# Kernel optimization log

Hardware: AMD Instinct MI355X
Metric: run time of the kernel (lower is better)

Reference implementation:

```python
import jax, jax.numpy as jnp
import numpy as np

NUM_STUDENTS = 50000
NUM_KP = 100
KD = 128          # knowledge_dim
HID = 256         # hidden_dim
B = 16384
K = 20            # max_knowledge_points


def setup_inputs() -> dict:
    key = jax.random.key(0)
    ks = jax.random.split(key, 16)
    inp = {
        "student_indices": jax.random.randint(ks[0], (B,), 0, NUM_STUDENTS, dtype=jnp.int32),
        "kp_indices": jax.random.randint(ks[1], (B, K), 0, NUM_KP, dtype=jnp.int32),
        "kp_lengths": jax.random.randint(ks[2], (B,), 0, K + 1, dtype=jnp.int32),
        # learned parameters
        "emb": jax.random.normal(ks[3], (NUM_STUDENTS, NUM_KP, KD), dtype=jnp.float32),
        # attention: Linear(KD,HID) -> tanh -> Linear(HID,1) -> softmax(dim=1)
        "W1": jax.random.normal(ks[4], (KD, HID), dtype=jnp.float32) * 0.05,
        "b1": jnp.zeros((HID,), jnp.float32),
        "w2": jax.random.normal(ks[5], (HID, 1), dtype=jnp.float32) * 0.05,
        "b2": jnp.zeros((1,), jnp.float32),
        # MLP: Linear(KD,HID)-ReLU-Linear(HID,HID//2)-ReLU-Linear(HID//2,1)-Sigmoid
        "M1": jax.random.normal(ks[6], (KD, HID), dtype=jnp.float32) * 0.05,
        "mb1": jnp.zeros((HID,), jnp.float32),
        "M2": jax.random.normal(ks[7], (HID, HID // 2), dtype=jnp.float32) * 0.05,
        "mb2": jnp.zeros((HID // 2,), jnp.float32),
        "M3": jax.random.normal(ks[8], (HID // 2, 1), dtype=jnp.float32) * 0.05,
        "mb3": jnp.zeros((1,), jnp.float32),
    }
    return inp


def reference(student_indices, kp_indices, kp_lengths, emb, W1, b1, w2, b2,
              M1, mb1, M2, mb2, M3, mb3):
    # ragged gather -> padded [B, K, KD]; padded slots are zero (as in the torch loop)
    vecs = emb[student_indices[:, None], kp_indices]            # [B,K,KD]
    mask = (jnp.arange(K)[None, :] < kp_lengths[:, None]).astype(vecs.dtype)  # [B,K]
    vecs = vecs * mask[:, :, None]
    # attention: Linear-Tanh-Linear-Softmax(dim=1), THEN masked (matches original order)
    logits = jnp.tanh(vecs @ W1 + b1) @ w2 + b2                 # [B,K,1]
    att = jax.nn.softmax(logits, axis=1) * mask[:, :, None]     # [B,K,1]
    weighted = jnp.sum(att * vecs, axis=1)                      # [B,KD]
    # MLP (dropout = identity in eval)
    h = jax.nn.relu(weighted @ M1 + mb1)
    h = jax.nn.relu(h @ M2 + mb2)
    scores = jax.nn.sigmoid(h @ M3 + mb3)[:, 0]                 # [B]
    return scores, att[:, :, 0]
```

## Files before the change

kernel.cpp:

```cpp
#include <hip/hip_runtime.h>
#include <hip/hip_bf16.h>

#define K_ 20
#define KD_ 128
#define HID_ 256
#define NKP_ 100

using short8_t = __attribute__((ext_vector_type(8))) short;
using f32x4 = __attribute__((ext_vector_type(4))) float;

__device__ __forceinline__ unsigned short f2bf(float f) {
    union { __hip_bfloat16 h; unsigned short u; } c; c.h = __float2bfloat16(f); return c.u;
}
__device__ __forceinline__ float vexp(float x) { float r; asm("v_exp_f32 %0, %1" : "=v"(r) : "v"(x)); return r; }
__device__ __forceinline__ float vrcp(float x) { float r; asm("v_rcp_f32 %0, %1" : "=v"(r) : "v"(x)); return r; }
__device__ __forceinline__ float bf_lo(unsigned u) { return __uint_as_float(u << 16); }
__device__ __forceinline__ float bf_hi(unsigned u) { return __uint_as_float(u & 0xffff0000u); }

#define CEXP 2.885390081777927f

__global__ __launch_bounds__(256) void prep_frags(
    const float* __restrict__ W1, const float* __restrict__ M1,
    const float* __restrict__ M2, unsigned short* __restrict__ w1f,
    unsigned short* __restrict__ m1f, unsigned short* __restrict__ m2f)
{
    const int b = blockIdx.x;
    const float* src; unsigned short* dst; int nc, smask, nshift, ib;
    if (b < 128)      { src = W1; dst = w1f; nc = 256; smask = 3; nshift = 2; ib = b; }
    else if (b < 256) { src = M1; dst = m1f; nc = 256; smask = 3; nshift = 2; ib = b - 128; }
    else              { src = M2; dst = m2f; nc = 128; smask = 7; nshift = 3; ib = b - 256; }
    const int i = ib * 256 + threadIdx.x;
    const int j = i & 7, l = (i >> 3) & 63, f = i >> 9;
    const int s = f & smask, n = f >> nshift;
    const int k = s * 32 + (l >> 4) * 8 + j;
    const int col = n * 16 + (l & 15);
    dst[i] = f2bf(src[k * nc + col]);
}

__global__ __launch_bounds__(256, 3) void cdm_attn(
    const int* __restrict__ stu_idx, const int* __restrict__ kp_idx,
    const int* __restrict__ kp_len, const float* __restrict__ emb,
    const unsigned short* __restrict__ w1f,
    const float* __restrict__ b1, const float* __restrict__ w2,
    const float* __restrict__ b2,
    float* __restrict__ out_att, unsigned short* __restrict__ wsum_g)
{
    const int tid = threadIdx.x, lane = tid & 63, w = tid >> 6;
    const int base = blockIdx.x * 8;

    __shared__ unsigned short vec_s[8][K_][KD_];
    __shared__ float lp_s[4][2][4][24];
    __shared__ float l0_s[4];
    __shared__ int   len_s[8];
    __shared__ float att_s[8][K_];

    const int g = lane >> 4, c16 = lane & 15;
    int lens[2]; long long eb[2]; int kpr[2][5];
#pragma unroll
    for (int h = 0; h < 2; ++h) {
        const int gs = base + 2 * w + h;
        lens[h] = kp_len[gs];
        eb[h] = (long long)stu_idx[gs] * (NKP_ * KD_);
#pragma unroll
        for (int it = 0; it < 5; ++it)
            kpr[h][it] = kp_idx[gs * K_ + it * 4 + g];
    }

    {
        float4 va[10], vb[10];
#pragma unroll
        for (int h = 0; h < 2; ++h) {
#pragma unroll
            for (int it = 0; it < 5; ++it) {
                const int q = h * 5 + it;
                va[q] = make_float4(0.f, 0.f, 0.f, 0.f);
                vb[q] = make_float4(0.f, 0.f, 0.f, 0.f);
                const int r = it * 4 + g;
                if (r < lens[h]) {
                    const float4* src = (const float4*)(emb + eb[h] + (long long)kpr[h][it] * KD_) + c16 * 2;
                    va[q] = src[0]; vb[q] = src[1];
                }
            }
        }
#pragma unroll
        for (int h = 0; h < 2; ++h) {
            char* sb = (char*)&vec_s[2 * w + h][0][0];
#pragma unroll
            for (int it = 0; it < 5; ++it) {
                const int q = h * 5 + it;
                const int r = it * 4 + g;
                short8_t pk;
                pk[0] = (short)f2bf(va[q].x); pk[1] = (short)f2bf(va[q].y);
                pk[2] = (short)f2bf(va[q].z); pk[3] = (short)f2bf(va[q].w);
                pk[4] = (short)f2bf(vb[q].x); pk[5] = (short)f2bf(vb[q].y);
                pk[6] = (short)f2bf(vb[q].z); pk[7] = (short)f2bf(vb[q].w);
                *(short8_t*)(sb + r * 256 + ((c16 * 16) ^ ((r & 7) << 4))) = pk;
            }
        }
        if (lane == 0) { len_s[2 * w] = lens[0]; len_s[2 * w + 1] = lens[1]; }
    }

    short8_t Bf[4][4];
    {
        const short8_t* bfr = (const short8_t*)w1f;
#pragma unroll
        for (int nn = 0; nn < 4; ++nn)
#pragma unroll
            for (int s = 0; s < 4; ++s)
                Bf[nn][s] = bfr[((w * 4 + nn) * 4 + s) * 64 + lane];
    }
    float b1C[4], w2r[4], n2r[4];
#pragma unroll
    for (int nn = 0; nn < 4; ++nn) {
        const int c = (w * 4 + nn) * 16 + (lane & 15);
        b1C[nn] = b1[c] * CEXP;
        w2r[nn] = w2[c];
        n2r[nn] = -2.f * w2r[nn];
    }
    const float b2v = b2[0];

    {
        float p = 0.f;
#pragma unroll
        for (int nn = 0; nn < 4; ++nn)
            p = fmaf(n2r[nn], vrcp(vexp(b1C[nn]) + 1.f), p + w2r[nn]);
#pragma unroll
        for (int m = 1; m <= 8; m <<= 1) p += __shfl_xor(p, m);
        if (lane == 0) l0_s[w] = p;
    }
    __syncthreads();
    const float logit0 = l0_s[0] + l0_s[1] + l0_s[2] + l0_s[3] + b2v;

#pragma unroll
    for (int p = 0; p < 4; ++p) {
        const int sp = 2 * p;
        const int lA = len_s[sp], lB = len_s[sp + 1];
        const bool need2 = (lA > 16) || (lB > 16);

        short8_t A0[4], A1[4];
        {
            const char* bA = (const char*)&vec_s[sp][0][0];
            const char* bB = (const char*)&vec_s[sp + 1][0][0];
            const int lr = lane & 15;
            const int rowb = lr * 256;
#pragma unroll
            for (int s = 0; s < 4; ++s) {
                const int colA = (s * 64 + (lane >> 4) * 16) ^ ((lr & 7) << 4);
                A0[s] = *(const short8_t*)(bA + rowb + colA);
                A1[s] = *(const short8_t*)(bB + rowb + colA);
            }
        }

        float lp0[4] = {0, 0, 0, 0}, lp1[4] = {0, 0, 0, 0};
#pragma unroll
        for (int nn = 0; nn < 4; ++nn) {
            f32x4 a0 = {0.f, 0.f, 0.f, 0.f}, a1 = {0.f, 0.f, 0.f, 0.f};
#pragma unroll
            for (int s = 0; s < 4; ++s) {
                a0 = __builtin_amdgcn_mfma_f32_16x16x32_bf16(A0[s], Bf[nn][s], a0, 0, 0, 0);
                a1 = __builtin_amdgcn_mfma_f32_16x16x32_bf16(A1[s], Bf[nn][s], a1, 0, 0, 0);
            }
            const float bc = b1C[nn], wv = w2r[nn], n2 = n2r[nn];
#pragma unroll
            for (int i = 0; i < 4; ++i) {
                lp0[i] = fmaf(n2, vrcp(vexp(fmaf(a0[i], CEXP, bc)) + 1.f), lp0[i] + wv);
                lp1[i] = fmaf(n2, vrcp(vexp(fmaf(a1[i], CEXP, bc)) + 1.f), lp1[i] + wv);
            }
        }
#pragma unroll
        for (int i = 0; i < 4; ++i) {
#pragma unroll
            for (int m = 1; m <= 8; m <<= 1) {
                lp0[i] += __shfl_xor(lp0[i], m);
                lp1[i] += __shfl_xor(lp1[i], m);
            }
        }
        if ((lane & 15) == 0) {
            const int gq = lane >> 4;
#pragma unroll
            for (int i = 0; i < 4; ++i) {
                lp_s[p][0][w][gq * 4 + i] = lp0[i];
                lp_s[p][1][w][gq * 4 + i] = lp1[i];
            }
        }

        if (need2) {
            short8_t A2[4];
            const int lr = lane & 15;
            const char* t2b = (const char*)&vec_s[sp + ((lr >> 2) & 1)][0][0] + (16 + (lr & 3)) * 256;
            const bool v2 = lr < 8;
            const short8_t z = {0, 0, 0, 0, 0, 0, 0, 0};
#pragma unroll
            for (int s = 0; s < 4; ++s) {
                const int colT = s * 64 + (lane >> 4) * 16;
                const short8_t t = *(const short8_t*)(t2b + (colT ^ ((lr & 3) << 4)));
                A2[s] = v2 ? t : z;
            }
            float lp2[4] = {0, 0, 0, 0};
#pragma unroll
            for (int nn = 0; nn < 4; ++nn) {
                f32x4 a2 = {0.f, 0.f, 0.f, 0.f};
#pragma unroll
                for (int s = 0; s < 4; ++s)
                    a2 = __builtin_amdgcn_mfma_f32_16x16x32_bf16(A2[s], Bf[nn][s], a2, 0, 0, 0);
                const float bc = b1C[nn], wv = w2r[nn], n2 = n2r[nn];
#pragma unroll
                for (int i = 0; i < 4; ++i)
                    lp2[i] = fmaf(n2, vrcp(vexp(fmaf(a2[i], CEXP, bc)) + 1.f), lp2[i] + wv);
            }
#pragma unroll
            for (int i = 0; i < 4; ++i) {
#pragma unroll
                for (int m = 1; m <= 8; m <<= 1) lp2[i] += __shfl_xor(lp2[i], m);
            }
            if ((lane & 15) == 0 && (lane >> 4) < 2) {
                const int gq = lane >> 4;
#pragma unroll
                for (int i = 0; i < 4; ++i) lp_s[p][gq][w][16 + i] = lp2[i];
            }
        }
    }
    __syncthreads();

    {
        const int j = lane & 31, hh = lane >> 5;
        const int smp = 2 * w + hh;
        const int gsS = base + smp;
        const int lenS = len_s[smp];
        float logit = -1e30f;
        if (j < K_) {
            logit = (j < lenS)
                ? b2v + lp_s[w][hh][0][j] + lp_s[w][hh][1][j]
                      + lp_s[w][hh][2][j] + lp_s[w][hh][3][j]
                : logit0;
        }
        float mx = logit;
#pragma unroll
        for (int m = 16; m >= 1; m >>= 1) mx = fmaxf(mx, __shfl_xor(mx, m, 32));
        const float e = (j < K_) ? vexp((logit - mx) * 1.44269504f) : 0.f;
        float sm = e;
#pragma unroll
        for (int m = 16; m >= 1; m >>= 1) sm += __shfl_xor(sm, m, 32);
        const float attv = (j < lenS) ? e * vrcp(sm) : 0.f;
        if (j < K_) { att_s[smp][j] = attv; out_att[gsS * K_ + j] = attv; }

        const int d0 = (lane & 31) * 4;
        const char* vb2 = (const char*)&vec_s[smp][0][0];
        const int lm = max(len_s[2 * w], len_s[2 * w + 1]);
        float s0 = 0.f, s1 = 0.f, s2 = 0.f, s3 = 0.f;
        for (int k = 0; k < lm; ++k) {
            const float av = att_s[smp][k];
            const uint2 u = *(const uint2*)(vb2 + k * 256 + ((2 * d0) ^ ((k & 7) << 4)));
            s0 = fmaf(av, bf_lo(u.x), s0);
            s1 = fmaf(av, bf_hi(u.x), s1);
            s2 = fmaf(av, bf_lo(u.y), s2);
            s3 = fmaf(av, bf_hi(u.y), s3);
        }
        uint2 pk;
        pk.x = (unsigned)f2bf(s0) | ((unsigned)f2bf(s1) << 16);
        pk.y = (unsigned)f2bf(s2) | ((unsigned)f2bf(s3) << 16);
        *(uint2*)(wsum_g + gsS * KD_ + d0) = pk;
    }
}

__global__ __launch_bounds__(512) void cdm_mlp(
    const unsigned short* __restrict__ wsum_g,
    const unsigned short* __restrict__ m1f, const unsigned short* __restrict__ m2f,
    const float* __restrict__ mb1, const float* __restrict__ mb2,
    const float* __restrict__ M3, const float* __restrict__ mb3,
    float* __restrict__ out_scores)
{
    const int tid = threadIdx.x, lane = tid & 63, w = tid >> 6;
    const int S0 = blockIdx.x * 32;
    const int lr = lane & 15, g = lane >> 4;

    __shared__ unsigned short h1_s[32][HID_];
    __shared__ float sc_s[8][32];

    short8_t Aw[2][4];
#pragma unroll
    for (int m = 0; m < 2; ++m)
#pragma unroll
        for (int s = 0; s < 4; ++s)
            Aw[m][s] = *(const short8_t*)(wsum_g + (S0 + m * 16 + lr) * KD_
                                          + s * 32 + g * 8);
    short8_t B1r[2][4];
    {
        const short8_t* bf1 = (const short8_t*)m1f;
#pragma unroll
        for (int nn = 0; nn < 2; ++nn)
#pragma unroll
            for (int s = 0; s < 4; ++s)
                B1r[nn][s] = bf1[((w * 2 + nn) * 4 + s) * 64 + lane];
    }
#pragma unroll
    for (int nn = 0; nn < 2; ++nn) {
        f32x4 c0 = {0.f, 0.f, 0.f, 0.f}, c1 = {0.f, 0.f, 0.f, 0.f};
#pragma unroll
        for (int s = 0; s < 4; ++s) {
            c0 = __builtin_amdgcn_mfma_f32_16x16x32_bf16(Aw[0][s], B1r[nn][s], c0, 0, 0, 0);
            c1 = __builtin_amdgcn_mfma_f32_16x16x32_bf16(Aw[1][s], B1r[nn][s], c1, 0, 0, 0);
        }
        const int col = (w * 2 + nn) * 16 + lr;
        const float bias = mb1[col];
#pragma unroll
        for (int i = 0; i < 4; ++i) {
            const int r0 = g * 4 + i;
            const int r1 = 16 + r0;
            *(unsigned short*)((char*)h1_s + r0 * 512 + ((2 * col) ^ ((r0 & 7) << 4)))
                = f2bf(fmaxf(c0[i] + bias, 0.f));
            *(unsigned short*)((char*)h1_s + r1 * 512 + ((2 * col) ^ ((r0 & 7) << 4)))
                = f2bf(fmaxf(c1[i] + bias, 0.f));
        }
    }
    __syncthreads();

    short8_t B2r[8];
    {
        const short8_t* bf2 = (const short8_t*)m2f;
#pragma unroll
        for (int s = 0; s < 8; ++s)
            B2r[s] = bf2[(w * 8 + s) * 64 + lane];
    }
    f32x4 d0 = {0.f, 0.f, 0.f, 0.f}, d1 = {0.f, 0.f, 0.f, 0.f};
#pragma unroll
    for (int s = 0; s < 8; ++s) {
        const int off = (s * 64 + g * 16) ^ ((lr & 7) << 4);
        const short8_t Ah0 = *(const short8_t*)((const char*)h1_s + lr * 512 + off);
        const short8_t Ah1 = *(const short8_t*)((const char*)h1_s + (16 + lr) * 512 + off);
        d0 = __builtin_amdgcn_mfma_f32_16x16x32_bf16(Ah0, B2r[s], d0, 0, 0, 0);
        d1 = __builtin_amdgcn_mfma_f32_16x16x32_bf16(Ah1, B2r[s], d1, 0, 0, 0);
    }
    {
        const int col = w * 16 + lr;
        const float bb = mb2[col], m3v = M3[col];
        float part0[4], part1[4];
#pragma unroll
        for (int i = 0; i < 4; ++i) {
            part0[i] = fmaxf(d0[i] + bb, 0.f) * m3v;
            part1[i] = fmaxf(d1[i] + bb, 0.f) * m3v;
        }
#pragma unroll
        for (int i = 0; i < 4; ++i) {
#pragma unroll
            for (int q = 1; q <= 8; q <<= 1) {
                part0[i] += __shfl_xor(part0[i], q);
                part1[i] += __shfl_xor(part1[i], q);
            }
        }
        if (lr == 0) {
#pragma unroll
            for (int i = 0; i < 4; ++i) {
                sc_s[w][g * 4 + i]      = part0[i];
                sc_s[w][16 + g * 4 + i] = part1[i];
            }
        }
    }
    __syncthreads();
    if (tid < 32) {
        const float sc = sc_s[0][tid] + sc_s[1][tid] + sc_s[2][tid] + sc_s[3][tid]
                       + sc_s[4][tid] + sc_s[5][tid] + sc_s[6][tid] + sc_s[7][tid] + mb3[0];
        out_scores[S0 + tid] = 1.f / (1.f + __expf(-sc));
    }
}

extern "C" void kernel_launch(void* const* d_in, const int* in_sizes, int n_in,
                              void* d_out, int out_size, void* d_ws, size_t ws_size,
                              hipStream_t stream) {
    const int*   stu = (const int*)d_in[0];
    const int*   kpi = (const int*)d_in[1];
    const int*   kpl = (const int*)d_in[2];
    const float* emb = (const float*)d_in[3];
    const float* W1  = (const float*)d_in[4];
    const float* b1  = (const float*)d_in[5];
    const float* w2  = (const float*)d_in[6];
    const float* b2  = (const float*)d_in[7];
    const float* M1  = (const float*)d_in[8];
    const float* mb1 = (const float*)d_in[9];
    const float* M2  = (const float*)d_in[10];
    const float* mb2 = (const float*)d_in[11];
    const float* M3  = (const float*)d_in[12];
    const float* mb3 = (const float*)d_in[13];
    const int B = in_sizes[0];

    float* out_scores = (float*)d_out;
    float* out_att    = out_scores + B;

    unsigned short* w1f  = (unsigned short*)d_ws;
    unsigned short* m1f  = w1f + 32768;
    unsigned short* m2f  = m1f + 32768;
    unsigned short* wsum = m2f + 32768;

    prep_frags<<<384, 256, 0, stream>>>(W1, M1, M2, w1f, m1f, m2f);
    cdm_attn<<<B / 8, 256, 0, stream>>>(stu, kpi, kpl, emb, w1f, b1, w2, b2,
                                        out_att, wsum);
    cdm_mlp<<<B / 32, 512, 0, stream>>>(wsum, m1f, m2f, mb1, mb2, M3, mb3, out_scores);
}
```

Measured before the change: 71.84 us.

## Halve students per attention block and assign one student per wave

The attention kernel now handles 4 students per 256-thread block instead of 8, so each wave gathers and owns a single student. The grid doubles and launch bounds rise to 4 blocks per CU, since shared memory use is halved. The weighted-sum stage now uses a full 64-lane wave per student and loops only up to that student's length instead of the pair maximum. The intent is more blocks in flight to hide gather latency and less wasted work. In exchange, each block reloads the W1 fragments and recomputes logit0 for half as many students, and there is less memory-level parallelism per wave.

```diff
diff --git a/kernel.cpp b/kernel.cpp
--- a/kernel.cpp
+++ b/kernel.cpp
@@ -37,7 +37,7 @@
     dst[i] = f2bf(src[k * nc + col]);
 }
 
-__global__ __launch_bounds__(256, 3) void cdm_attn(
+__global__ __launch_bounds__(256, 4) void cdm_attn(
     const int* __restrict__ stu_idx, const int* __restrict__ kp_idx,
     const int* __restrict__ kp_len, const float* __restrict__ emb,
     const unsigned short* __restrict__ w1f,
@@ -46,58 +46,47 @@
     float* __restrict__ out_att, unsigned short* __restrict__ wsum_g)
 {
     const int tid = threadIdx.x, lane = tid & 63, w = tid >> 6;
-    const int base = blockIdx.x * 8;
-
-    __shared__ unsigned short vec_s[8][K_][KD_];
-    __shared__ float lp_s[4][2][4][24];
+    const int base = blockIdx.x * 4;
+
+    __shared__ unsigned short vec_s[4][K_][KD_];
+    __shared__ float lp_s[2][2][4][24];
     __shared__ float l0_s[4];
-    __shared__ int   len_s[8];
-    __shared__ float att_s[8][K_];
+    __shared__ int   len_s[4];
+    __shared__ float att_s[4][K_];
 
     const int g = lane >> 4, c16 = lane & 15;
-    int lens[2]; long long eb[2]; int kpr[2][5];
-#pragma unroll
-    for (int h = 0; h < 2; ++h) {
-        const int gs = base + 2 * w + h;
-        lens[h] = kp_len[gs];
-        eb[h] = (long long)stu_idx[gs] * (NKP_ * KD_);
-#pragma unroll
-        for (int it = 0; it < 5; ++it)
-            kpr[h][it] = kp_idx[gs * K_ + it * 4 + g];
-    }
-
-    {
-        float4 va[10], vb[10];
-#pragma unroll
-        for (int h = 0; h < 2; ++h) {
-#pragma unroll
-            for (int it = 0; it < 5; ++it) {
-                const int q = h * 5 + it;
-                va[q] = make_float4(0.f, 0.f, 0.f, 0.f);
-                vb[q] = make_float4(0.f, 0.f, 0.f, 0.f);
-                const int r = it * 4 + g;
-                if (r < lens[h]) {
-                    const float4* src = (const float4*)(emb + eb[h] + (long long)kpr[h][it] * KD_) + c16 * 2;
-                    va[q] = src[0]; vb[q] = src[1];
-                }
-            }
-        }
-#pragma unroll
-        for (int h = 0; h < 2; ++h) {
-            char* sb = (char*)&vec_s[2 * w + h][0][0];
-#pragma unroll
-            for (int it = 0; it < 5; ++it) {
-                const int q = h * 5 + it;
-                const int r = it * 4 + g;
-                short8_t pk;
-                pk[0] = (short)f2bf(va[q].x); pk[1] = (short)f2bf(va[q].y);
-                pk[2] = (short)f2bf(va[q].z); pk[3] = (short)f2bf(va[q].w);
-                pk[4] = (short)f2bf(vb[q].x); pk[5] = (short)f2bf(vb[q].y);
-                pk[6] = (short)f2bf(vb[q].z); pk[7] = (short)f2bf(vb[q].w);
-                *(short8_t*)(sb + r * 256 + ((c16 * 16) ^ ((r & 7) << 4))) = pk;
-            }
-        }
-        if (lane == 0) { len_s[2 * w] = lens[0]; len_s[2 * w + 1] = lens[1]; }
+    const int gs = base + w;
+    const int len = kp_len[gs];
+    const long long eb = (long long)stu_idx[gs] * (NKP_ * KD_);
+    int kpr[5];
+#pragma unroll
+    for (int it = 0; it < 5; ++it)
+        kpr[it] = kp_idx[gs * K_ + it * 4 + g];
+
+    {
+        float4 va[5], vb[5];
+#pragma unroll
+        for (int it = 0; it < 5; ++it) {
+            va[it] = make_float4(0.f, 0.f, 0.f, 0.f);
+            vb[it] = make_float4(0.f, 0.f, 0.f, 0.f);
+            const int r = it * 4 + g;
+            if (r < len) {
+                const float4* src = (const float4*)(emb + eb + (long long)kpr[it] * KD_) + c16 * 2;
+                va[it] = src[0]; vb[it] = src[1];
+            }
+        }
+        char* sb = (char*)&vec_s[w][0][0];
+#pragma unroll
+        for (int it = 0; it < 5; ++it) {
+            const int r = it * 4 + g;
+            short8_t pk;
+            pk[0] = (short)f2bf(va[it].x); pk[1] = (short)f2bf(va[it].y);
+            pk[2] = (short)f2bf(va[it].z); pk[3] = (short)f2bf(va[it].w);
+            pk[4] = (short)f2bf(vb[it].x); pk[5] = (short)f2bf(vb[it].y);
+            pk[6] = (short)f2bf(vb[it].z); pk[7] = (short)f2bf(vb[it].w);
+            *(short8_t*)(sb + r * 256 + ((c16 * 16) ^ ((r & 7) << 4))) = pk;
+        }
+        if (lane == 0) len_s[w] = len;
     }
 
     short8_t Bf[4][4];
@@ -132,7 +121,7 @@
     const float logit0 = l0_s[0] + l0_s[1] + l0_s[2] + l0_s[3] + b2v;
 
 #pragma unroll
-    for (int p = 0; p < 4; ++p) {
+    for (int p = 0; p < 2; ++p) {
         const int sp = 2 * p;
         const int lA = len_s[sp], lB = len_s[sp + 1];
         const bool need2 = (lA > 16) || (lB > 16);
@@ -223,43 +212,35 @@
     __syncthreads();
 
     {
-        const int j = lane & 31, hh = lane >> 5;
-        const int smp = 2 * w + hh;
-        const int gsS = base + smp;
-        const int lenS = len_s[smp];
+        const int p = w >> 1, hh = w & 1;
+        const int lenS = len_s[w];
         float logit = -1e30f;
-        if (j < K_) {
-            logit = (j < lenS)
-                ? b2v + lp_s[w][hh][0][j] + lp_s[w][hh][1][j]
-                      + lp_s[w][hh][2][j] + lp_s[w][hh][3][j]
+        if (lane < K_) {
+            logit = (lane < lenS)
+                ? b2v + lp_s[p][hh][0][lane] + lp_s[p][hh][1][lane]
+                      + lp_s[p][hh][2][lane] + lp_s[p][hh][3][lane]
                 : logit0;
         }
         float mx = logit;
 #pragma unroll
-        for (int m = 16; m >= 1; m >>= 1) mx = fmaxf(mx, __shfl_xor(mx, m, 32));
-        const float e = (j < K_) ? vexp((logit - mx) * 1.44269504f) : 0.f;
+        for (int m = 32; m >= 1; m >>= 1) mx = fmaxf(mx, __shfl_xor(mx, m));
+        const float e = (lane < K_) ? vexp((logit - mx) * 1.44269504f) : 0.f;
         float sm = e;
 #pragma unroll
-        for (int m = 16; m >= 1; m >>= 1) sm += __shfl_xor(sm, m, 32);
-        const float attv = (j < lenS) ? e * vrcp(sm) : 0.f;
-        if (j < K_) { att_s[smp][j] = attv; out_att[gsS * K_ + j] = attv; }
-
-        const int d0 = (lane & 31) * 4;
-        const char* vb2 = (const char*)&vec_s[smp][0][0];
-        const int lm = max(len_s[2 * w], len_s[2 * w + 1]);
-        float s0 = 0.f, s1 = 0.f, s2 = 0.f, s3 = 0.f;
-        for (int k = 0; k < lm; ++k) {
-            const float av = att_s[smp][k];
-            const uint2 u = *(const uint2*)(vb2 + k * 256 + ((2 * d0) ^ ((k & 7) << 4)));
-            s0 = fmaf(av, bf_lo(u.x), s0);
-            s1 = fmaf(av, bf_hi(u.x), s1);
-            s2 = fmaf(av, bf_lo(u.y), s2);
-            s3 = fmaf(av, bf_hi(u.y), s3);
-        }
-        uint2 pk;
-        pk.x = (unsigned)f2bf(s0) | ((unsigned)f2bf(s1) << 16);
-        pk.y = (unsigned)f2bf(s2) | ((unsigned)f2bf(s3) << 16);
-        *(uint2*)(wsum_g + gsS * KD_ + d0) = pk;
+        for (int m = 32; m >= 1; m >>= 1) sm += __shfl_xor(sm, m);
+        const float attv = (lane < lenS) ? e * vrcp(sm) : 0.f;
+        if (lane < K_) { att_s[w][lane] = attv; out_att[gs * K_ + lane] = attv; }
+
+        const char* vb2 = (const char*)&vec_s[w][0][0];
+        float s0 = 0.f, s1 = 0.f;
+        for (int k = 0; k < lenS; ++k) {
+            const float av = att_s[w][k];
+            const unsigned u = *(const unsigned*)(vb2 + k * 256 + ((lane * 4) ^ ((k & 7) << 4)));
+            s0 = fmaf(av, bf_lo(u), s0);
+            s1 = fmaf(av, bf_hi(u), s1);
+        }
+        const unsigned pk = (unsigned)f2bf(s0) | ((unsigned)f2bf(s1) << 16);
+        *(unsigned*)(wsum_g + gs * KD_ + lane * 2) = pk;
     }
 }
 
@@ -392,7 +373,7 @@
     unsigned short* wsum = m2f + 32768;
 
     prep_frags<<<384, 256, 0, stream>>>(W1, M1, M2, w1f, m1f, m2f);
-    cdm_attn<<<B / 8, 256, 0, stream>>>(stu, kpi, kpl, emb, w1f, b1, w2, b2,
+    cdm_attn<<<B / 4, 256, 0, stream>>>(stu, kpi, kpl, emb, w1f, b1, w2, b2,
                                         out_att, wsum);
     cdm_mlp<<<B / 32, 512, 0, stream>>>(wsum, m1f, m2f, mb1, mb2, M3, mb3, out_scores);
 }
```

After: 97.65 us. +35.9%, slower.
